# Performance work log

Measured on AMD Instinct MI355X. Metric: run time of the kernel, lower is better.

## Reference

```python
import jax, jax.numpy as jnp
import numpy as np

DIM = 128
IN_DIM = 2
LAYERS = 4
H = 256
W = 256
WH = W // 2 + 1  # rfft last-dim size
RATIO = 1.0


def _radial_mask():
    # waves = sqrt(k^2 + r^2) over the rfft2 grid; keep waves <= (W//2)*ratio
    k = np.fft.rfftfreq(W) * W            # (WH,)
    r = np.fft.fftfreq(H) * H             # (H,)
    waves = np.sqrt(k[None, :] ** 2 + r[:, None] ** 2)  # (H, WH)
    return jnp.asarray(waves <= (W // 2) * RATIO)


def conv1x1(x, w, b):
    # x: (b,c,h,w), w: (o,c), b: (o,)
    return jnp.einsum('bchw,oc->bohw', x, w) + b[None, :, None, None]


def setup_inputs() -> dict:
    key = jax.random.key(0)
    ks = jax.random.split(key, 15)
    d = DIM
    inp = {
        'x': jax.random.normal(ks[0], (4, IN_DIM, H, W), dtype=jnp.float32),
        'enc_w': jax.random.normal(ks[1], (d, IN_DIM), dtype=jnp.float32) * (1.0 / np.sqrt(IN_DIM)),
        'enc_b': jnp.zeros((d,), dtype=jnp.float32),
        'pos_emb': jax.random.normal(ks[2], (1, d, H, W), dtype=jnp.float32) * 0.02,
        'mlp_w1': jax.random.normal(ks[3], (LAYERS, 4 * d, d), dtype=jnp.float32) * (1.0 / np.sqrt(d)),
        'mlp_b1': jnp.zeros((LAYERS, 4 * d), dtype=jnp.float32),
        'mlp_w2': jax.random.normal(ks[4], (LAYERS, d, 4 * d), dtype=jnp.float32) * (1.0 / np.sqrt(4 * d)),
        'mlp_b2': jnp.zeros((LAYERS, d), dtype=jnp.float32),
        'spec_mags': jax.random.normal(ks[5], (LAYERS, d, H, WH), dtype=jnp.float32),
        'spec_phases': jax.random.normal(ks[6], (LAYERS, d, H, WH), dtype=jnp.float32),
        'oxo_w': jax.random.normal(ks[7], (LAYERS, d, d), dtype=jnp.float32) * (1.0 / np.sqrt(d)),
        'oxo_b': jnp.zeros((LAYERS, d), dtype=jnp.float32),
        'dec_w': jax.random.normal(ks[8], (IN_DIM, d), dtype=jnp.float32) * (1.0 / np.sqrt(d)),
        'dec_b': jnp.zeros((IN_DIM,), dtype=jnp.float32),
    }
    return inp


def reference(x, enc_w, enc_b, pos_emb, mlp_w1, mlp_b1, mlp_w2, mlp_b2,
              spec_mags, spec_phases, oxo_w, oxo_b, dec_w, dec_b):
    scale = (DIM / IN_DIM) ** 0.5
    mask = _radial_mask()  # (H, WH) bool, constant
    h = conv1x1(x, enc_w, enc_b) * scale + pos_emb
    for i in range(LAYERS):
        # mlp block: 1x1 conv -> SiLU -> 1x1 conv
        x1 = jax.nn.silu(conv1x1(h, mlp_w1[i], mlp_b1[i]))
        x1 = conv1x1(x1, mlp_w2[i], mlp_b2[i])
        # spectral conv: rfft2 (ortho), complex filter on radially-masked modes,
        # zeros elsewhere (equivalent to masked_select/scatter in the original), irfft2
        xf = jnp.fft.rfft2(x1, norm='ortho')  # (b,c,H,WH) complex64
        filt = jax.nn.sigmoid(spec_mags[i]) * jnp.exp(1j * spec_phases[i])  # (c,H,WH)
        xf = jnp.where(mask[None, None, :, :], xf * filt[None], 0.0 + 0.0j)
        x1 = jnp.fft.irfft2(xf, s=(H, W), norm='ortho')
        x1 = conv1x1(x1, oxo_w[i], oxo_b[i])
        h = x1 + h
    return conv1x1(h, dec_w, dec_b) / scale
```

## Files before the change

kernel.cpp:

```cpp
#include <hip/hip_runtime.h>
#include <math.h>

#define PI2 6.2831853071795864769f

typedef short bf16x8 __attribute__((ext_vector_type(8)));
typedef float f32x4 __attribute__((ext_vector_type(4)));
typedef int   i32x4 __attribute__((ext_vector_type(4)));

__device__ inline unsigned splitf(float v) {
    unsigned u  = __float_as_uint(v);
    unsigned r  = (u + 0x7fffu + ((u >> 16) & 1u)) >> 16;
    float hi    = __uint_as_float(r << 16);
    float lof   = v - hi;
    unsigned u2 = __float_as_uint(lof);
    unsigned r2 = (u2 + 0x7fffu + ((u2 >> 16) & 1u)) >> 16;
    return (r & 0xffffu) | (r2 << 16);
}
__device__ inline float upk(unsigned w) {
    return __uint_as_float(w << 16) + __uint_as_float(w & 0xffff0000u);
}

union VecU { i32x4 i; bf16x8 s; };

__device__ inline void unpack2(i32x4 d0, i32x4 d1, bf16x8& hi, bf16x8& lo) {
    VecU h, l;
    h.i.x = __builtin_amdgcn_perm(d0.y, d0.x, 0x05040100);
    h.i.y = __builtin_amdgcn_perm(d0.w, d0.z, 0x05040100);
    h.i.z = __builtin_amdgcn_perm(d1.y, d1.x, 0x05040100);
    h.i.w = __builtin_amdgcn_perm(d1.w, d1.z, 0x05040100);
    l.i.x = __builtin_amdgcn_perm(d0.y, d0.x, 0x07060302);
    l.i.y = __builtin_amdgcn_perm(d0.w, d0.z, 0x07060302);
    l.i.z = __builtin_amdgcn_perm(d1.y, d1.x, 0x07060302);
    l.i.w = __builtin_amdgcn_perm(d1.w, d1.z, 0x07060302);
    hi = h.s; lo = l.s;
}

__device__ inline void unpack8(const int* d, bf16x8& hi, bf16x8& lo) {
    VecU h, l;
    h.i.x = __builtin_amdgcn_perm(d[1], d[0], 0x05040100);
    h.i.y = __builtin_amdgcn_perm(d[3], d[2], 0x05040100);
    h.i.z = __builtin_amdgcn_perm(d[5], d[4], 0x05040100);
    h.i.w = __builtin_amdgcn_perm(d[7], d[6], 0x05040100);
    l.i.x = __builtin_amdgcn_perm(d[1], d[0], 0x07060302);
    l.i.y = __builtin_amdgcn_perm(d[3], d[2], 0x07060302);
    l.i.z = __builtin_amdgcn_perm(d[5], d[4], 0x07060302);
    l.i.w = __builtin_amdgcn_perm(d[7], d[6], 0x07060302);
    hi = h.s; lo = l.s;
}

__global__ void sentinel_kernel(float* __restrict__ out, int n) {
    int t = blockIdx.x * 256 + threadIdx.x;
    if (t < n) out[t] = 12345.0f;
}

__global__ void split_kernel(const float* __restrict__ in, unsigned* __restrict__ out) {
    long q = (long)blockIdx.x * 256 + threadIdx.x;
    const float4* ip = (const float4*)in;
    float4 v = ip[q];
    i32x4 o;
    o.x = (int)splitf(v.x); o.y = (int)splitf(v.y);
    o.z = (int)splitf(v.z); o.w = (int)splitf(v.w);
    ((i32x4*)out)[q] = o;
}

__global__ void enc_kernel(const float* __restrict__ x, const float* __restrict__ w,
                           const float* __restrict__ b, const float* __restrict__ pos,
                           unsigned* __restrict__ h) {
    long t = (long)blockIdx.x * 256 + threadIdx.x;
    int pq = (int)(t & 16383);
    int c  = (int)((t >> 14) & 127);
    int bb = (int)(t >> 21);
    float4 x0 = *(const float4*)(x + ((long)bb * 2 + 0) * 65536 + pq * 4);
    float4 x1 = *(const float4*)(x + ((long)bb * 2 + 1) * 65536 + pq * 4);
    float4 pv = *(const float4*)(pos + (long)c * 65536 + pq * 4);
    float w0 = w[c * 2], w1 = w[c * 2 + 1], bc = b[c];
    uint4 o;
    o.x = splitf((w0 * x0.x + w1 * x1.x + bc) * 8.0f + pv.x);
    o.y = splitf((w0 * x0.y + w1 * x1.y + bc) * 8.0f + pv.y);
    o.z = splitf((w0 * x0.z + w1 * x1.z + bc) * 8.0f + pv.z);
    o.w = splitf((w0 * x0.w + w1 * x1.w + bc) * 8.0f + pv.w);
    *(uint4*)(h + t * 4) = o;
}

__global__ __launch_bounds__(256, 1)
void mlp_fused(const unsigned* __restrict__ Ax, const unsigned* __restrict__ W1x,
               const float* __restrict__ b1, const unsigned* __restrict__ W2x,
               const float* __restrict__ b2, float* __restrict__ t2) {
    __shared__ unsigned LB[8704];
    int tid = threadIdx.x;
    int w = tid >> 6, l = tid & 63;
    int lr = l & 15, lg = l >> 4;
    int p0 = blockIdx.x * 64;

    unsigned apk[4][4][8];
#pragma unroll
    for (int ms = 0; ms < 4; ms++)
#pragma unroll
        for (int ks = 0; ks < 4; ks++) {
            const unsigned* ap = Ax + (long)(ks * 32 + lg * 8) * 65536 + p0 + ms * 16 + lr;
#pragma unroll
            for (int j = 0; j < 8; j++) apk[ms][ks][j] = ap[(long)j * 65536];
        }

    f32x4 acc2[4][2] = {};
#pragma unroll 1
    for (int c = 0; c < 4; c++) {
        f32x4 acc1[4][2] = {};
#pragma unroll
        for (int ks = 0; ks < 4; ks++) {
            bf16x8 bh[2], bl[2];
#pragma unroll
            for (int ns = 0; ns < 2; ns++) {
                const unsigned* bp = W1x + (c * 128 + w * 32 + ns * 16 + lr) * 128 + ks * 32 + lg * 8;
                i32x4 d0 = *(const i32x4*)bp;
                i32x4 d1 = *(const i32x4*)(bp + 4);
                unpack2(d0, d1, bh[ns], bl[ns]);
            }
#pragma unroll
            for (int ms = 0; ms < 4; ms++) {
                bf16x8 ah, al; unpack8((const int*)apk[ms][ks], ah, al);
#pragma unroll
                for (int ns = 0; ns < 2; ns++) {
                    acc1[ms][ns] = __builtin_amdgcn_mfma_f32_16x16x32_bf16(ah, bh[ns], acc1[ms][ns], 0, 0, 0);
                    acc1[ms][ns] = __builtin_amdgcn_mfma_f32_16x16x32_bf16(ah, bl[ns], acc1[ms][ns], 0, 0, 0);
                    acc1[ms][ns] = __builtin_amdgcn_mfma_f32_16x16x32_bf16(al, bh[ns], acc1[ms][ns], 0, 0, 0);
                }
            }
        }
#pragma unroll
        for (int ns = 0; ns < 2; ns++) {
            int hdl = w * 32 + ns * 16 + lr;
            float bias = b1[c * 128 + hdl];
#pragma unroll
            for (int ms = 0; ms < 4; ms++)
#pragma unroll
                for (int r = 0; r < 4; r++) {
                    float pre = acc1[ms][ns][r] + bias;
                    float s = pre / (1.0f + __expf(-pre));
                    int pix = ms * 16 + lg * 4 + r;
                    LB[pix * 132 + hdl] = splitf(s);
                }
        }
        __syncthreads();
#pragma unroll
        for (int ks2 = 0; ks2 < 4; ks2++) {
            bf16x8 bh[2], bl[2];
#pragma unroll
            for (int ns = 0; ns < 2; ns++) {
                const unsigned* bp = W2x + (w * 32 + ns * 16 + lr) * 512 + c * 128 + ks2 * 32 + lg * 8;
                i32x4 d0 = *(const i32x4*)bp;
                i32x4 d1 = *(const i32x4*)(bp + 4);
                unpack2(d0, d1, bh[ns], bl[ns]);
            }
#pragma unroll
            for (int ms = 0; ms < 4; ms++) {
                const i32x4* hp = (const i32x4*)&LB[(ms * 16 + lr) * 132 + ks2 * 32 + lg * 8];
                i32x4 d0 = hp[0], d1 = hp[1];
                bf16x8 ah, al; unpack2(d0, d1, ah, al);
#pragma unroll
                for (int ns = 0; ns < 2; ns++) {
                    acc2[ms][ns] = __builtin_amdgcn_mfma_f32_16x16x32_bf16(ah, bh[ns], acc2[ms][ns], 0, 0, 0);
                    acc2[ms][ns] = __builtin_amdgcn_mfma_f32_16x16x32_bf16(ah, bl[ns], acc2[ms][ns], 0, 0, 0);
                    acc2[ms][ns] = __builtin_amdgcn_mfma_f32_16x16x32_bf16(al, bh[ns], acc2[ms][ns], 0, 0, 0);
                }
            }
        }
        __syncthreads();
    }
    float* T = (float*)LB;
#pragma unroll
    for (int ns = 0; ns < 2; ns++) {
        int n = w * 32 + ns * 16 + lr;
        float bias = b2[n];
#pragma unroll
        for (int ms = 0; ms < 4; ms++)
#pragma unroll
            for (int r = 0; r < 4; r++) {
                int pix = ms * 16 + lg * 4 + r;
                T[n * 68 + pix] = acc2[ms][ns][r] + bias;
            }
    }
    __syncthreads();
#pragma unroll
    for (int i = 0; i < 8; i++) {
        int f = i * 256 + tid;
        int n = f >> 4, q = f & 15;
        float4 v = *(const float4*)&T[n * 68 + q * 4];
        *(float4*)(t2 + (long)n * 65536 + p0 + q * 4) = v;
    }
}

__global__ __launch_bounds__(256, 2)
void oxo_kernel(const unsigned* __restrict__ Tx, const unsigned* __restrict__ Bx,
                const float* __restrict__ ob, unsigned* __restrict__ h) {
    __shared__ float T[128 * 128];
    int tid = threadIdx.x;
    int w = tid >> 6, l = tid & 63;
    int lr = l & 15, lg = l >> 4;
    int m0 = blockIdx.x * 128;
    int n0 = w * 32;
    f32x4 acc[8][2] = {};
    for (int k0 = 0; k0 < 128; k0 += 32) {
        bf16x8 bh[2], bl[2];
#pragma unroll
        for (int ns = 0; ns < 2; ns++) {
            const unsigned* bp = Bx + (n0 + ns * 16 + lr) * 128 + k0 + lg * 8;
            i32x4 d0 = *(const i32x4*)bp;
            i32x4 d1 = *(const i32x4*)(bp + 4);
            unpack2(d0, d1, bh[ns], bl[ns]);
        }
#pragma unroll
        for (int ms = 0; ms < 8; ms++) {
            const unsigned* ap = Tx + (long)(k0 + lg * 8) * 65536 + m0 + ms * 16 + lr;
            int d[8];
#pragma unroll
            for (int j = 0; j < 8; j++) d[j] = (int)ap[(long)j * 65536];
            bf16x8 ah, al; unpack8(d, ah, al);
#pragma unroll
            for (int ns = 0; ns < 2; ns++) {
                acc[ms][ns] = __builtin_amdgcn_mfma_f32_16x16x32_bf16(ah, bh[ns], acc[ms][ns], 0, 0, 0);
                acc[ms][ns] = __builtin_amdgcn_mfma_f32_16x16x32_bf16(ah, bl[ns], acc[ms][ns], 0, 0, 0);
                acc[ms][ns] = __builtin_amdgcn_mfma_f32_16x16x32_bf16(al, bh[ns], acc[ms][ns], 0, 0, 0);
            }
        }
    }
#pragma unroll
    for (int ns = 0; ns < 2; ns++) {
        int n = n0 + ns * 16 + lr;
#pragma unroll
        for (int ms = 0; ms < 8; ms++) {
            int blk = ((ms * 4 + lg) + n) & 31;
#pragma unroll
            for (int r = 0; r < 4; r++)
                T[n * 128 + blk * 4 + r] = acc[ms][ns][r];
        }
    }
    __syncthreads();
#pragma unroll
    for (int i = 0; i < 16; i++) {
        int flat = i * 256 + tid;
        int n = flat >> 5, q = flat & 31;
        const float4* src = (const float4*)&T[n * 128 + (((q + n) & 31) * 4)];
        float4 v = *src;
        float bias = ob[n];
        unsigned* hp = h + (long)n * 65536 + m0 + q * 4;
        uint4 hv = *(uint4*)hp;
        uint4 o;
        o.x = splitf(upk(hv.x) + v.x + bias);
        o.y = splitf(upk(hv.y) + v.y + bias);
        o.z = splitf(upk(hv.z) + v.z + bias);
        o.w = splitf(upk(hv.w) + v.w + bias);
        *(uint4*)hp = o;
    }
}

__global__ void fft_row_fwd(const float* __restrict__ in, float2* __restrict__ freq, int c0) {
    __shared__ float2 A[4][256];
    __shared__ float2 B[4][256];
    __shared__ float2 TW[128];
    int tid = threadIdx.x;
    int img = blockIdx.x >> 6, rgrp = blockIdx.x & 63;
    if (tid < 128) {
        float sn, cs; __sincosf((PI2 / 256.f) * (float)tid, &sn, &cs);
        TW[tid] = make_float2(cs, sn);
    }
    {
        int r = tid >> 6, l = tid & 63;
        const float4* src = (const float4*)(in + ((long)(c0 + img) * 256 + rgrp * 4 + r) * 256);
        float4 v = src[l];
        A[r][l * 4 + 0] = make_float2(v.x, 0.f);
        A[r][l * 4 + 1] = make_float2(v.y, 0.f);
        A[r][l * 4 + 2] = make_float2(v.z, 0.f);
        A[r][l * 4 + 3] = make_float2(v.w, 0.f);
    }
    __syncthreads();
    float2 (*s)[256] = A; float2 (*d)[256] = B;
    for (int m = 1; m < 256; m <<= 1) {
#pragma unroll
        for (int q = 0; q < 2; q++) {
            int bf = tid + q * 256;
            int r = bf >> 7, i = bf & 127;
            int jm = i & ~(m - 1);
            float2 c0v = s[r][i], c1 = s[r][i + 128];
            float2 t = TW[jm];
            float2 df = make_float2(c0v.x - c1.x, c0v.y - c1.y);
            d[r][i + jm]     = make_float2(c0v.x + c1.x, c0v.y + c1.y);
            d[r][i + jm + m] = make_float2(t.x * df.x + t.y * df.y, t.x * df.y - t.y * df.x);
        }
        __syncthreads();
        float2 (*tmp)[256] = s; s = d; d = tmp;
    }
    long ib = (long)img * 34816;
    for (int q = tid; q < 4 * 129; q += 256) {
        int r = q / 129; int k = q - r * 129;
        freq[ib + (k >> 3) * 2048 + (rgrp * 4 + r) * 8 + (k & 7)] = s[r][k];
    }
}

__global__ void fft_col(float2* __restrict__ freq, const float* __restrict__ mags,
                        const float* __restrict__ phases, int c0) {
    __shared__ float2 A[8][256];
    __shared__ float2 B[8][256];
    __shared__ float2 TW[128];
    int tid = threadIdx.x;
    int img = blockIdx.x / 17;
    int kt  = blockIdx.x % 17;
    int kx0 = kt * 8;
    float2* base = freq + (long)img * 34816 + kt * 2048;
    if (tid < 128) {
        float sn, cs; __sincosf((PI2 / 256.f) * (float)tid, &sn, &cs);
        TW[tid] = make_float2(cs, sn);
    }
#pragma unroll
    for (int q = 0; q < 8; q++) {
        int e = tid + q * 256;
        A[e & 7][e >> 3] = base[e];
    }
    __syncthreads();
    float2 (*s)[256] = A; float2 (*d)[256] = B;
    for (int m = 1; m < 256; m <<= 1) {
#pragma unroll
        for (int q = 0; q < 4; q++) {
            int bf = tid + q * 256;
            int cl = bf >> 7, i = bf & 127;
            int jm = i & ~(m - 1);
            float2 c0v = s[cl][i], c1 = s[cl][i + 128];
            float2 t = TW[jm];
            float2 df = make_float2(c0v.x - c1.x, c0v.y - c1.y);
            d[cl][i + jm]     = make_float2(c0v.x + c1.x, c0v.y + c1.y);
            d[cl][i + jm + m] = make_float2(t.x * df.x + t.y * df.y, t.x * df.y - t.y * df.x);
        }
        __syncthreads();
        float2 (*tmp)[256] = s; s = d; d = tmp;
    }
#pragma unroll
    for (int q = 0; q < 8; q++) {
        int e = tid + q * 256;
        int cl = e & 7, ky = e >> 3;
        int kx = kx0 + cl;
        float2 v = s[cl][ky];
        float2 r = make_float2(0.f, 0.f);
        if (kx < 129) {
            int ry = ky < 128 ? ky : ky - 256;
            if (kx * kx + ry * ry <= 16384) {
                long fi = ((long)(c0 + img) * 256 + ky) * 129 + kx;
                float mg = mags[fi], ph = phases[fi];
                float sg = 1.0f / (1.0f + __expf(-mg));
                float sn, cs; __sincosf(ph, &sn, &cs);
                float fr = sg * cs, fim = sg * sn;
                r = make_float2(v.x * fr - v.y * fim, v.x * fim + v.y * fr);
            }
        }
        s[cl][ky] = r;
    }
    __syncthreads();
    for (int m = 1; m < 256; m <<= 1) {
#pragma unroll
        for (int q = 0; q < 4; q++) {
            int bf = tid + q * 256;
            int cl = bf >> 7, i = bf & 127;
            int jm = i & ~(m - 1);
            float2 c0v = s[cl][i], c1 = s[cl][i + 128];
            float2 t = TW[jm];
            float2 df = make_float2(c0v.x - c1.x, c0v.y - c1.y);
            d[cl][i + jm]     = make_float2(c0v.x + c1.x, c0v.y + c1.y);
            d[cl][i + jm + m] = make_float2(t.x * df.x - t.y * df.y, t.x * df.y + t.y * df.x);
        }
        __syncthreads();
        float2 (*tmp)[256] = s; s = d; d = tmp;
    }
#pragma unroll
    for (int q = 0; q < 8; q++) {
        int e = tid + q * 256;
        base[e] = s[e & 7][e >> 3];
    }
}

__global__ void fft_row_inv(const float2* __restrict__ freq, unsigned* __restrict__ out, int c0) {
    __shared__ float2 A[4][256];
    __shared__ float2 B[4][256];
    __shared__ float2 TW[128];
    int tid = threadIdx.x;
    int img = blockIdx.x >> 6, rgrp = blockIdx.x & 63;
    if (tid < 128) {
        float sn, cs; __sincosf((PI2 / 256.f) * (float)tid, &sn, &cs);
        TW[tid] = make_float2(cs, sn);
    }
    long ib = (long)img * 34816;
#pragma unroll
    for (int q = 0; q < 4; q++) {
        int e = tid + q * 256;
        int r = e >> 8, xx = e & 255;
        int k = (xx <= 128) ? xx : 256 - xx;
        float2 v = freq[ib + (k >> 3) * 2048 + (rgrp * 4 + r) * 8 + (k & 7)];
        if (xx > 128) v.y = -v.y;
        A[r][xx] = v;
    }
    __syncthreads();
    float2 (*s)[256] = A; float2 (*d)[256] = B;
    for (int m = 1; m < 256; m <<= 1) {
#pragma unroll
        for (int q = 0; q < 2; q++) {
            int bf = tid + q * 256;
            int r = bf >> 7, i = bf & 127;
            int jm = i & ~(m - 1);
            float2 c0v = s[r][i], c1 = s[r][i + 128];
            float2 t = TW[jm];
            float2 df = make_float2(c0v.x - c1.x, c0v.y - c1.y);
            d[r][i + jm]     = make_float2(c0v.x + c1.x, c0v.y + c1.y);
            d[r][i + jm + m] = make_float2(t.x * df.x - t.y * df.y, t.x * df.y + t.y * df.x);
        }
        __syncthreads();
        float2 (*tmp)[256] = s; s = d; d = tmp;
    }
    {
        int r = tid >> 6, l = tid & 63;
        const float sc = 1.0f / 65536.0f;
        uint4 o;
        o.x = splitf(s[r][l * 4 + 0].x * sc);
        o.y = splitf(s[r][l * 4 + 1].x * sc);
        o.z = splitf(s[r][l * 4 + 2].x * sc);
        o.w = splitf(s[r][l * 4 + 3].x * sc);
        *(uint4*)(out + ((long)(c0 + img) * 256 + rgrp * 4 + r) * 256 + l * 4) = o;
    }
}

__global__ void dec_kernel(const unsigned* __restrict__ h, const float* __restrict__ w,
                           const float* __restrict__ b, float* __restrict__ out) {
    int t = blockIdx.x * 256 + threadIdx.x;
    int bb = t >> 16, p = t & 65535;
    const unsigned* hb = h + (long)bb * 8388608 + p;
    float a0 = b[0], a1 = b[1];
    float a0b = 0.f, a1b = 0.f;
#pragma unroll 4
    for (int c = 0; c < 128; c += 2) {
        float h0 = upk(hb[(long)c * 65536]);
        float h1 = upk(hb[(long)(c + 1) * 65536]);
        a0  += w[c] * h0;        a1  += w[128 + c] * h0;
        a0b += w[c + 1] * h1;    a1b += w[128 + c + 1] * h1;
    }
    out[((long)bb * 2 + 0) * 65536 + p] = (a0 + a0b) * 0.125f;
    out[((long)bb * 2 + 1) * 65536 + p] = (a1 + a1b) * 0.125f;
}

extern "C" void kernel_launch(void* const* d_in, const int* in_sizes, int n_in,
                              void* d_out, int out_size, void* d_ws, size_t ws_size,
                              hipStream_t stream) {
    const float* x        = (const float*)d_in[0];
    const float* enc_w    = (const float*)d_in[1];
    const float* enc_b    = (const float*)d_in[2];
    const float* pos_emb  = (const float*)d_in[3];
    const float* mlp_w1   = (const float*)d_in[4];
    const float* mlp_b1   = (const float*)d_in[5];
    const float* mlp_w2   = (const float*)d_in[6];
    const float* mlp_b2   = (const float*)d_in[7];
    const float* spec_mag = (const float*)d_in[8];
    const float* spec_ph  = (const float*)d_in[9];
    const float* oxo_w    = (const float*)d_in[10];
    const float* oxo_b    = (const float*)d_in[11];
    const float* dec_w    = (const float*)d_in[12];
    const float* dec_b    = (const float*)d_in[13];
    float* outp = (float*)d_out;

    const size_t WS_NEEDED = 186187776ULL;
    if (ws_size < WS_NEEDED) {
        sentinel_kernel<<<(out_size + 255) / 256, 256, 0, stream>>>(outp, out_size);
        return;
    }

    unsigned* u    = (unsigned*)d_ws;
    unsigned* h    = u;
    float*    t2   = (float*)(u + 33554432);
    unsigned* TxO  = (unsigned*)t2;
    float2*   freq = (float2*)(u + 41943040);
    unsigned* Wx1  = u + 46399488;
    unsigned* Wx2  = Wx1 + 65536;
    unsigned* Wox  = Wx2 + 65536;

    enc_kernel<<<32768, 256, 0, stream>>>(x, enc_w, enc_b, pos_emb, h);

    for (int l = 0; l < 4; l++) {
        split_kernel<<<64, 256, 0, stream>>>(mlp_w1 + (long)l * 65536, Wx1);
        split_kernel<<<64, 256, 0, stream>>>(mlp_w2 + (long)l * 65536, Wx2);
        split_kernel<<<16, 256, 0, stream>>>(oxo_w + (long)l * 16384, Wox);
        const float* b1l = mlp_b1 + l * 512;
        const float* b2l = mlp_b2 + l * 128;
        const float* mgl = spec_mag + (long)l * 4227072;
        const float* phl = spec_ph  + (long)l * 4227072;
        const float* obl = oxo_b + l * 128;
        for (int b = 0; b < 4; b++) {
            unsigned* hb = h + (long)b * 8388608;
            mlp_fused<<<1024, 256, 0, stream>>>(hb, Wx1, b1l, Wx2, b2l, t2);
            for (int c0 = 0; c0 < 128; c0 += 64) {
                fft_row_fwd<<<4096, 256, 0, stream>>>(t2, freq, c0);
                fft_col<<<64 * 17, 256, 0, stream>>>(freq, mgl, phl, c0);
                fft_row_inv<<<4096, 256, 0, stream>>>(freq, TxO, c0);
            }
            oxo_kernel<<<512, 256, 0, stream>>>(TxO, Wox, obl, hb);
        }
    }

    dec_kernel<<<1024, 256, 0, stream>>>(h, dec_w, dec_b, outp);
}
```

Baseline: 4.343 ms.

## Stage MLP input tile in LDS and halve hidden chunk to raise occupancy

The fused MLP kernel used to keep the whole 64-pixel by 128-channel input tile in registers (128 packed words per thread). It now loads that tile into LDS once with coalesced uint4 reads and a transpose, and reads A fragments from LDS on every k-step. The hidden dimension is processed in 8 chunks of 64 instead of 4 chunks of 128, so each wave keeps fewer accumulators. Together these cut register pressure enough to request 2 blocks per CU, in exchange for more LDS traffic, more barriers, and a larger shared footprint.

```diff
diff --git a/kernel.cpp b/kernel.cpp
--- a/kernel.cpp
+++ b/kernel.cpp
@@ -82,79 +82,80 @@
     *(uint4*)(h + t * 4) = o;
 }
 
-__global__ __launch_bounds__(256, 1)
+__global__ __launch_bounds__(256, 2)
 void mlp_fused(const unsigned* __restrict__ Ax, const unsigned* __restrict__ W1x,
                const float* __restrict__ b1, const unsigned* __restrict__ W2x,
                const float* __restrict__ b2, float* __restrict__ t2) {
-    __shared__ unsigned LB[8704];
+    __shared__ unsigned SM[12800];
+    unsigned* ALDS = SM;
+    unsigned* HLDS = SM + 8448;
     int tid = threadIdx.x;
     int w = tid >> 6, l = tid & 63;
     int lr = l & 15, lg = l >> 4;
     int p0 = blockIdx.x * 64;
 
-    unsigned apk[4][4][8];
-#pragma unroll
-    for (int ms = 0; ms < 4; ms++)
-#pragma unroll
-        for (int ks = 0; ks < 4; ks++) {
-            const unsigned* ap = Ax + (long)(ks * 32 + lg * 8) * 65536 + p0 + ms * 16 + lr;
-#pragma unroll
-            for (int j = 0; j < 8; j++) apk[ms][ks][j] = ap[(long)j * 65536];
-        }
+#pragma unroll
+    for (int i = 0; i < 8; i++) {
+        int f = i * 256 + tid;
+        int k = f >> 4, q = f & 15;
+        uint4 v = *(const uint4*)(Ax + (long)k * 65536 + p0 + q * 4);
+        ALDS[(q * 4 + 0) * 132 + k] = v.x;
+        ALDS[(q * 4 + 1) * 132 + k] = v.y;
+        ALDS[(q * 4 + 2) * 132 + k] = v.z;
+        ALDS[(q * 4 + 3) * 132 + k] = v.w;
+    }
+    __syncthreads();
 
     f32x4 acc2[4][2] = {};
 #pragma unroll 1
-    for (int c = 0; c < 4; c++) {
-        f32x4 acc1[4][2] = {};
+    for (int c = 0; c < 8; c++) {
+        f32x4 acc1[4] = {};
 #pragma unroll
         for (int ks = 0; ks < 4; ks++) {
+            bf16x8 bh, bl;
+            {
+                const unsigned* bp = W1x + (c * 64 + w * 16 + lr) * 128 + ks * 32 + lg * 8;
+                i32x4 d0 = *(const i32x4*)bp;
+                i32x4 d1 = *(const i32x4*)(bp + 4);
+                unpack2(d0, d1, bh, bl);
+            }
+#pragma unroll
+            for (int ms = 0; ms < 4; ms++) {
+                const i32x4* apx = (const i32x4*)&ALDS[(ms * 16 + lr) * 132 + ks * 32 + lg * 8];
+                i32x4 a0 = apx[0], a1 = apx[1];
+                bf16x8 ah, al; unpack2(a0, a1, ah, al);
+                acc1[ms] = __builtin_amdgcn_mfma_f32_16x16x32_bf16(ah, bh, acc1[ms], 0, 0, 0);
+                acc1[ms] = __builtin_amdgcn_mfma_f32_16x16x32_bf16(ah, bl, acc1[ms], 0, 0, 0);
+                acc1[ms] = __builtin_amdgcn_mfma_f32_16x16x32_bf16(al, bh, acc1[ms], 0, 0, 0);
+            }
+        }
+        {
+            int hl = w * 16 + lr;
+            float bias = b1[c * 64 + hl];
+#pragma unroll
+            for (int ms = 0; ms < 4; ms++)
+#pragma unroll
+                for (int r = 0; r < 4; r++) {
+                    float pre = acc1[ms][r] + bias;
+                    float s = pre / (1.0f + __expf(-pre));
+                    int pix = ms * 16 + lg * 4 + r;
+                    HLDS[pix * 68 + hl] = splitf(s);
+                }
+        }
+        __syncthreads();
+#pragma unroll
+        for (int ks2 = 0; ks2 < 2; ks2++) {
             bf16x8 bh[2], bl[2];
 #pragma unroll
             for (int ns = 0; ns < 2; ns++) {
-                const unsigned* bp = W1x + (c * 128 + w * 32 + ns * 16 + lr) * 128 + ks * 32 + lg * 8;
+                const unsigned* bp = W2x + (w * 32 + ns * 16 + lr) * 512 + c * 64 + ks2 * 32 + lg * 8;
                 i32x4 d0 = *(const i32x4*)bp;
                 i32x4 d1 = *(const i32x4*)(bp + 4);
                 unpack2(d0, d1, bh[ns], bl[ns]);
             }
 #pragma unroll
             for (int ms = 0; ms < 4; ms++) {
-                bf16x8 ah, al; unpack8((const int*)apk[ms][ks], ah, al);
-#pragma unroll
-                for (int ns = 0; ns < 2; ns++) {
-                    acc1[ms][ns] = __builtin_amdgcn_mfma_f32_16x16x32_bf16(ah, bh[ns], acc1[ms][ns], 0, 0, 0);
-                    acc1[ms][ns] = __builtin_amdgcn_mfma_f32_16x16x32_bf16(ah, bl[ns], acc1[ms][ns], 0, 0, 0);
-                    acc1[ms][ns] = __builtin_amdgcn_mfma_f32_16x16x32_bf16(al, bh[ns], acc1[ms][ns], 0, 0, 0);
-                }
-            }
-        }
-#pragma unroll
-        for (int ns = 0; ns < 2; ns++) {
-            int hdl = w * 32 + ns * 16 + lr;
-            float bias = b1[c * 128 + hdl];
-#pragma unroll
-            for (int ms = 0; ms < 4; ms++)
-#pragma unroll
-                for (int r = 0; r < 4; r++) {
-                    float pre = acc1[ms][ns][r] + bias;
-                    float s = pre / (1.0f + __expf(-pre));
-                    int pix = ms * 16 + lg * 4 + r;
-                    LB[pix * 132 + hdl] = splitf(s);
-                }
-        }
-        __syncthreads();
-#pragma unroll
-        for (int ks2 = 0; ks2 < 4; ks2++) {
-            bf16x8 bh[2], bl[2];
-#pragma unroll
-            for (int ns = 0; ns < 2; ns++) {
-                const unsigned* bp = W2x + (w * 32 + ns * 16 + lr) * 512 + c * 128 + ks2 * 32 + lg * 8;
-                i32x4 d0 = *(const i32x4*)bp;
-                i32x4 d1 = *(const i32x4*)(bp + 4);
-                unpack2(d0, d1, bh[ns], bl[ns]);
-            }
-#pragma unroll
-            for (int ms = 0; ms < 4; ms++) {
-                const i32x4* hp = (const i32x4*)&LB[(ms * 16 + lr) * 132 + ks2 * 32 + lg * 8];
+                const i32x4* hp = (const i32x4*)&HLDS[(ms * 16 + lr) * 68 + ks2 * 32 + lg * 8];
                 i32x4 d0 = hp[0], d1 = hp[1];
                 bf16x8 ah, al; unpack2(d0, d1, ah, al);
 #pragma unroll
@@ -167,7 +168,7 @@
         }
         __syncthreads();
     }
-    float* T = (float*)LB;
+    float* T = (float*)SM;
 #pragma unroll
     for (int ns = 0; ns < 2; ns++) {
         int n = w * 32 + ns * 16 + lr;
```

Measured after the change: 3.996 ms. 1.09x faster.
